# Kernel tuning notes

Measured on AMD Instinct MI355X. Metric: run time of the kernel, lower is better.

Reference implementation:

```python
import jax, jax.numpy as jnp
import numpy as np

CHAN = 24
INNER = 64
GROUPS = 8
M = 5
LAM = 1e-4
MAX_ITER = 25
BETA = 1.0
EPS = 1e-5
B, HH, WW = 128, 32, 32


def conv2d(x, w, b=None):
    # NCHW, OIHW, 3x3 SAME conv (padding = kernel//2)
    y = jax.lax.conv_general_dilated(x, w, (1, 1), 'SAME',
                                     dimension_numbers=('NCHW', 'OIHW', 'NCHW'))
    if b is not None:
        y = y + b[None, :, None, None]
    return y


def group_norm(x, g, b):
    bsz, c, h, w = x.shape
    xg = x.reshape(bsz, GROUPS, c // GROUPS, h, w)
    mu = xg.mean(axis=(2, 3, 4), keepdims=True)
    var = xg.var(axis=(2, 3, 4), keepdims=True)
    xn = ((xg - mu) / jnp.sqrt(var + EPS)).reshape(bsz, c, h, w)
    return xn * g[None, :, None, None] + b[None, :, None, None]


def batch_norm(x, g, b):
    # training-mode batch statistics over (N, H, W)
    mu = x.mean(axis=(0, 2, 3), keepdims=True)
    var = x.var(axis=(0, 2, 3), keepdims=True)
    return (x - mu) / jnp.sqrt(var + EPS) * g[None, :, None, None] + b[None, :, None, None]


def resnet_f(p, z, x):
    c1w, g1g, g1b, c2w, g2g, g2b, g3g, g3b = p
    y = group_norm(jax.nn.relu(conv2d(z, c1w)), g1g, g1b)
    return group_norm(jax.nn.relu(z + group_norm(x + conv2d(y, c2w), g2g, g2b)), g3g, g3b)


def anderson(f, x0):
    # Anderson acceleration, fixed MAX_ITER iterations (no host-sync tol break).
    bsz = x0.shape[0]
    d = x0.size // bsz
    X = jnp.zeros((bsz, M, d), x0.dtype)
    Fm = jnp.zeros((bsz, M, d), x0.dtype)
    f0 = f(x0).reshape(bsz, -1)
    X = X.at[:, 0].set(x0.reshape(bsz, -1))
    Fm = Fm.at[:, 0].set(f0)
    X = X.at[:, 1].set(f0)
    Fm = Fm.at[:, 1].set(f(f0.reshape(x0.shape)).reshape(bsz, -1))
    for k in range(2, MAX_ITER):
        n = min(k, M)
        G = Fm[:, :n] - X[:, :n]                       # [b, n, d]
        Hm = jnp.zeros((bsz, n + 1, n + 1), x0.dtype)
        Hm = Hm.at[:, 0, 1:].set(1.0).at[:, 1:, 0].set(1.0)
        Hm = Hm.at[:, 1:, 1:].set(jnp.einsum('bnd,bmd->bnm', G, G)
                                  + LAM * jnp.eye(n, dtype=x0.dtype)[None])
        yv = jnp.zeros((bsz, n + 1, 1), x0.dtype).at[:, 0, 0].set(1.0)
        alpha = jnp.linalg.solve(Hm, yv)[:, 1:, 0]     # [b, n]
        xnew = (BETA * jnp.einsum('bn,bnd->bd', alpha, Fm[:, :n])
                + (1.0 - BETA) * jnp.einsum('bn,bnd->bd', alpha, X[:, :n]))
        X = X.at[:, k % M].set(xnew)
        Fm = Fm.at[:, k % M].set(f(xnew.reshape(x0.shape)).reshape(bsz, -1))
    return X[:, (MAX_ITER - 1) % M].reshape(x0.shape)


def setup_inputs() -> dict:
    key = jax.random.key(0)
    ks = jax.random.split(key, 8)
    inp = {
        'x': jax.random.normal(ks[0], (B, 3, HH, WW), jnp.float32),
        'pre_conv_w': jax.random.normal(ks[1], (CHAN, 3, 3, 3), jnp.float32) * 0.1,
        'pre_conv_b': jnp.zeros((CHAN,), jnp.float32),
        'pre_bn_g': jnp.ones((CHAN,), jnp.float32),
        'pre_bn_b': jnp.zeros((CHAN,), jnp.float32),
        'f_conv1_w': jax.random.normal(ks[2], (INNER, CHAN, 3, 3), jnp.float32) * 0.01,
        'gn1_g': jnp.ones((INNER,), jnp.float32),
        'gn1_b': jnp.zeros((INNER,), jnp.float32),
        'f_conv2_w': jax.random.normal(ks[3], (CHAN, INNER, 3, 3), jnp.float32) * 0.01,
        'gn2_g': jnp.ones((CHAN,), jnp.float32),
        'gn2_b': jnp.zeros((CHAN,), jnp.float32),
        'gn3_g': jnp.ones((CHAN,), jnp.float32),
        'gn3_b': jnp.zeros((CHAN,), jnp.float32),
        'post_bn_g': jnp.ones((CHAN,), jnp.float32),
        'post_bn_b': jnp.zeros((CHAN,), jnp.float32),
        'fc_w': jax.random.normal(ks[4], (10, CHAN * 4 * 4), jnp.float32) * 0.05,
        'fc_b': jnp.zeros((10,), jnp.float32),
    }
    return inp


def reference(x, pre_conv_w, pre_conv_b, pre_bn_g, pre_bn_b,
              f_conv1_w, gn1_g, gn1_b, f_conv2_w, gn2_g, gn2_b, gn3_g, gn3_b,
              post_bn_g, post_bn_b, fc_w, fc_b):
    # pre: conv + BatchNorm
    xp = batch_norm(conv2d(x, pre_conv_w, pre_conv_b), pre_bn_g, pre_bn_b)
    p = (f_conv1_w, gn1_g, gn1_b, f_conv2_w, gn2_g, gn2_b, gn3_g, gn3_b)
    # DEQ fixed-point solve (eval path: train=False returns the fixed point)
    z_star = anderson(lambda z: resnet_f(p, z, xp), jnp.zeros_like(xp))
    z = resnet_f(p, z_star, xp)
    # post: relu -> BN -> avgpool(8,8) -> flatten -> linear
    h = batch_norm(jax.nn.relu(z), post_bn_g, post_bn_b)
    bsz, c, hh, ww = h.shape
    pooled = h.reshape(bsz, c, hh // 8, 8, ww // 8, 8).mean(axis=(3, 5))  # [B,C,4,4]
    return pooled.reshape(bsz, -1) @ fc_w.T + fc_b
```

## Files before the change

### kernel.cpp

```cpp
#include <hip/hip_runtime.h>
#include <hip/hip_bf16.h>

typedef __hip_bfloat16 bf16;
typedef unsigned short ushortT;
typedef __attribute__((ext_vector_type(8))) short short8;
typedef __attribute__((ext_vector_type(4))) float f32x4;

#define BB 128
#define CHAN 24
#define INNER 64
#define HW 1024
#define DD (CHAN*HW)

constexpr size_t cBD = (size_t)BB*DD;
constexpr size_t cYB = (size_t)BB*INNER*HW;

__device__ __attribute__((aligned(16))) ushortT g_xp[cBD];
__device__ __attribute__((aligned(16))) ushortT g_X[5*cBD];
__device__ __attribute__((aligned(16))) ushortT g_F[5*cBD];
__device__ __attribute__((aligned(16))) ushortT g_G[5*cBD];
__device__ __attribute__((aligned(16))) ushortT g_yb[cYB];
__device__ __attribute__((aligned(16))) ushortT g_tb[cBD];
__device__ __attribute__((aligned(16))) ushortT g_w1m[9*64*32];
__device__ __attribute__((aligned(16))) ushortT g_w2m[9*24*64];
__device__ __attribute__((aligned(16))) float g_stats2a[48];
__device__ __attribute__((aligned(16))) float g_stats2b[48];
__device__ __attribute__((aligned(16))) float g_gn1sum[BB*8*2];
__device__ __attribute__((aligned(16))) float g_gn2sum[BB*24*2];
__device__ __attribute__((aligned(16))) float g_gn3p[BB*4*16];
__device__ __attribute__((aligned(16))) float g_gramp[BB*4*5*5];
__device__ __attribute__((aligned(16))) float g_gram[BB*25];
__device__ __attribute__((aligned(16))) float g_pooled[BB*CHAN*16];
__device__ __attribute__((aligned(16))) float g_params[5120];
__device__ unsigned g_isbf16;

#define P_PCW 0
#define P_PCB 648
#define P_PBG 672
#define P_PBB 696
#define P_G1G 720
#define P_G1B 784
#define P_G2G 848
#define P_G2B 872
#define P_G3G 896
#define P_G3B 920
#define P_POG 944
#define P_POB 968
#define P_FCW 992
#define P_FCB 4832

__device__ __forceinline__ float rdin(const void* p, int i){
  if (g_isbf16) return __bfloat162float(((const bf16*)p)[i]);
  return ((const float*)p)[i];
}
__device__ __forceinline__ float b2f(ushortT u){
  unsigned v = ((unsigned)u) << 16;
  return __builtin_bit_cast(float, v);
}
__device__ __forceinline__ ushortT f2b(float f){
  unsigned u = __builtin_bit_cast(unsigned, f);
  u += 0x7FFFu + ((u >> 16) & 1u);
  return (ushortT)(u >> 16);
}
__device__ __forceinline__ void ld24(const ushortT* p, float* o){
  short8 a = *(const short8*)p, b8 = *(const short8*)(p+8), c8 = *(const short8*)(p+16);
  #pragma unroll
  for (int j=0;j<8;j++){ o[j]=b2f((ushortT)a[j]); o[8+j]=b2f((ushortT)b8[j]); o[16+j]=b2f((ushortT)c8[j]); }
}
__device__ __forceinline__ void st24(ushortT* p, const float* i){
  short8 a,b8,c8;
  #pragma unroll
  for (int j=0;j<8;j++){ a[j]=(short)f2b(i[j]); b8[j]=(short)f2b(i[8+j]); c8[j]=(short)f2b(i[16+j]); }
  *(short8*)p = a; *(short8*)(p+8) = b8; *(short8*)(p+16) = c8;
}

__global__ void detect_k(const void* g1g){
  if (threadIdx.x==0 && blockIdx.x==0){
    unsigned u = *(const unsigned*)g1g;
    g_isbf16 = (u == 0x3F803F80u) ? 1u : 0u;
  }
}

__global__ void cvt_params_k(const void* pcw, const void* pcb, const void* pbg, const void* pbb,
                             const void* g1g, const void* g1b, const void* g2g, const void* g2b,
                             const void* g3g, const void* g3b, const void* pog, const void* pob,
                             const void* fcw, const void* fcb){
  int t = threadIdx.x;
  for (int i=t;i<648;i+=256)  g_params[P_PCW+i]=rdin(pcw,i);
  for (int i=t;i<24;i+=256) { g_params[P_PCB+i]=rdin(pcb,i);
                              g_params[P_PBG+i]=rdin(pbg,i);
                              g_params[P_PBB+i]=rdin(pbb,i);
                              g_params[P_G2G+i]=rdin(g2g,i);
                              g_params[P_G2B+i]=rdin(g2b,i);
                              g_params[P_G3G+i]=rdin(g3g,i);
                              g_params[P_G3B+i]=rdin(g3b,i);
                              g_params[P_POG+i]=rdin(pog,i);
                              g_params[P_POB+i]=rdin(pob,i); }
  for (int i=t;i<64;i+=256) { g_params[P_G1G+i]=rdin(g1g,i);
                              g_params[P_G1B+i]=rdin(g1b,i); }
  for (int i=t;i<3840;i+=256) g_params[P_FCW+i]=rdin(fcw,i);
  for (int i=t;i<10;i+=256)   g_params[P_FCB+i]=rdin(fcb,i);
  for (int i=t;i<48;i+=256) { g_stats2a[i]=0.f; g_stats2b[i]=0.f; }
}

__global__ void wtm_k(const void* w1, const void* w2){
  int t = blockIdx.x*256 + threadIdx.x;
  if (t < 9*64*32){
    int ic = t & 31, oc = (t>>5)&63, s9 = t>>11;
    float v = (ic<24) ? rdin(w1, (oc*24+ic)*9 + s9) : 0.f;
    g_w1m[t] = f2b(v);
  }
  int u = t - 9*64*32;
  if (u >= 0 && u < 9*24*64){
    int ic = u & 63; int rest = u >> 6; int oc = rest % 24; int s9 = rest / 24;
    g_w2m[u] = f2b(rdin(w2, (oc*64+ic)*9 + s9));
  }
}

__global__ void zeroX0_k(){
  size_t i = ((size_t)blockIdx.x*256 + threadIdx.x)*8;
  short8 z = {0,0,0,0,0,0,0,0};
  *(short8*)&g_X[i] = z;
  if (blockIdx.x < 8) g_gn1sum[blockIdx.x*256 + threadIdx.x] = 0.f;
}
__global__ void copyF0toX1_k(){
  size_t i = ((size_t)blockIdx.x*256 + threadIdx.x)*8;
  *(short8*)&g_X[cBD + i] = *(const short8*)&g_F[i];
  if (blockIdx.x < 8) g_gn1sum[blockIdx.x*256 + threadIdx.x] = 0.f;
}

__global__ void preconv_k(const void* __restrict__ x){
  int id = blockIdx.x*256 + threadIdx.x;
  int b = id >> 10, pix = id & 1023;
  int yy = pix >> 5, xx = pix & 31;
  float acc[24];
  #pragma unroll
  for (int oc=0;oc<24;oc++) acc[oc] = g_params[P_PCB+oc];
  for (int ic=0; ic<3; ic++)
    for (int ky=0; ky<3; ky++){
      int gy = yy+ky-1; if (gy<0||gy>=32) continue;
      for (int kx=0;kx<3;kx++){
        int gx = xx+kx-1; if (gx<0||gx>=32) continue;
        float v = rdin(x, ((b*3+ic)*32+gy)*32+gx);
        #pragma unroll
        for (int oc=0;oc<24;oc++)
          acc[oc] += v * g_params[P_PCW+(oc*3+ic)*9+ky*3+kx];
      }
    }
  st24(g_tb + (size_t)id*24, acc);
}

template<bool RELU>
__global__ void bnstat2_k(int which){
  const ushortT* src = (which==0) ? g_tb : (g_F + 4*cBD);
  float* dst = (which==0) ? g_stats2a : g_stats2b;
  __shared__ float sRed[48];
  int b = blockIdx.x >> 2, seg = blockIdx.x & 3;
  int t = threadIdx.x;
  if (t < 48) sRed[t] = 0.f;
  __syncthreads();
  int c8 = t % 3, pl = t / 3;
  float p0[8], p1[8];
  #pragma unroll
  for (int e=0;e<8;e++){ p0[e]=0.f; p1[e]=0.f; }
  for (int it=0; it<4; it++){
    int pix = seg*256 + it*64 + pl;
    short8 v = *(const short8*)&src[((size_t)b*1024 + pix)*24 + c8*8];
    #pragma unroll
    for (int e=0;e<8;e++){
      float f = b2f((ushortT)v[e]); if (RELU) f = fmaxf(f,0.f);
      p0[e]+=f; p1[e]+=f*f;
    }
  }
  #pragma unroll
  for (int e=0;e<8;e++){
    atomicAdd(&sRed[(c8*8+e)*2],   p0[e]);
    atomicAdd(&sRed[(c8*8+e)*2+1], p1[e]);
  }
  __syncthreads();
  if (t < 48) atomicAdd(&dst[t], sRed[t]);
}

__global__ void bn_apply_k(){
  int id = blockIdx.x*256+threadIdx.x;
  const float inv = 1.f/(BB*HW);
  float tv[24], ov[24];
  ld24(g_tb + (size_t)id*24, tv);
  #pragma unroll
  for (int c=0;c<24;c++){
    float mean = g_stats2a[c*2]*inv;
    float var = fmaxf(g_stats2a[c*2+1]*inv - mean*mean, 0.f);
    float rstd = rsqrtf(var + 1e-5f);
    ov[c] = (tv[c]-mean)*rstd*g_params[P_PBG+c] + g_params[P_PBB+c];
  }
  st24(g_xp + (size_t)id*24, ov);
}

__launch_bounds__(256, 2)
__global__ void conv1_k(int s){
  __shared__ ushortT sMem[29312];
  ushortT* sA = sMem;
  ushortT* sW = sMem + 10880;
  const int tid = threadIdx.x;
  const int lane = tid & 63, wv = tid >> 6;
  const int mLane = lane & 15, q = lane >> 4;
  const int b = blockIdx.x >> 2, yt = blockIdx.x & 3;
  const ushortT* __restrict__ Xs = g_X + (size_t)s*cBD;
  if (blockIdx.x < 24) g_gn2sum[blockIdx.x*256 + tid] = 0.f;
  for (int i = tid; i < 1360; i += 256){
    int icv = i & 3, apix = i >> 2;
    int yl = apix / 34, xl = apix - yl*34;
    int gy = yt*8 - 1 + yl, gx = xl - 1;
    short8 v = {0,0,0,0,0,0,0,0};
    if (gy >= 0 && gy < 32 && gx >= 0 && gx < 32 && icv < 3)
      v = *(const short8*)&Xs[((size_t)b*1024 + gy*32 + gx)*24 + icv*8];
    *(short8*)&sA[(size_t)(apix*4 + (icv ^ (apix&3)))*8] = v;
  }
  for (int i = tid; i < 2304; i += 256){
    int icv = i & 3, rest = i >> 2;
    int oc = rest & 63, s9 = rest >> 6;
    short8 v = *(const short8*)&g_w1m[(size_t)((s9*64 + oc)*32) + icv*8];
    *(short8*)&sW[(size_t)((s9*64+oc)*4 + (icv ^ (oc&3)))*8] = v;
  }
  __syncthreads();
  f32x4 acc[4][4];
  #pragma unroll
  for (int mt=0;mt<4;mt++)
    #pragma unroll
    for (int nt=0;nt<4;nt++) acc[mt][nt] = (f32x4){0.f,0.f,0.f,0.f};
  for (int s9=0; s9<9; s9++){
    int ky = s9/3, kx = s9 - ky*3;
    short8 bfr[4];
    #pragma unroll
    for (int nt=0;nt<4;nt++){
      int oc = nt*16 + mLane;
      bfr[nt] = *(const short8*)&sW[(size_t)((s9*64+oc)*4 + (q ^ (oc&3)))*8];
    }
    #pragma unroll
    for (int mt=0;mt<4;mt++){
      int g = wv*4+mt;
      int apix = ((g>>1) + ky)*34 + (g&1)*16 + mLane + kx;
      short8 afr = *(const short8*)&sA[(size_t)(apix*4 + (q ^ (apix&3)))*8];
      #pragma unroll
      for (int nt=0;nt<4;nt++)
        acc[mt][nt] = __builtin_amdgcn_mfma_f32_16x16x32_bf16(afr, bfr[nt], acc[mt][nt], 0,0,0);
    }
  }
  __syncthreads();
  ushortT* sOut = sMem;
  #pragma unroll
  for (int mt=0;mt<4;mt++){
    int g = wv*4+mt;
    #pragma unroll
    for (int nt=0;nt<4;nt++){
      int oc = nt*16 + mLane;
      #pragma unroll
      for (int r=0;r<4;r++){
        int pix = (g>>1)*32 + (g&1)*16 + q*4 + r;
        sOut[pix*64 + oc] = f2b(fmaxf(acc[mt][nt][r], 0.f));
      }
    }
  }
  __syncthreads();
  float s0=0.f, s1=0.f;
  size_t gbase = ((size_t)b*1024 + yt*256)*64;
  for (int c = tid; c < 2048; c += 256){
    short8 v = *(const short8*)&sOut[c*8];
    *(short8*)&g_yb[gbase + (size_t)c*8] = v;
    #pragma unroll
    for (int j=0;j<8;j++){ float f = b2f((ushortT)v[j]); s0 += f; s1 += f*f; }
  }
  s0 += __shfl_down(s0,32); s1 += __shfl_down(s1,32);
  s0 += __shfl_down(s0,16); s1 += __shfl_down(s1,16);
  s0 += __shfl_down(s0, 8); s1 += __shfl_down(s1, 8);
  if (lane < 8){
    atomicAdd(&g_gn1sum[(b*8+lane)*2],   s0);
    atomicAdd(&g_gn1sum[(b*8+lane)*2+1], s1);
  }
}

__launch_bounds__(256, 2)
__global__ void conv2_k(){
  __shared__ ushortT sMem[35584];
  __shared__ float sAff[128];
  ushortT* sA = sMem;
  ushortT* sW = sMem + 21760;
  const int tid = threadIdx.x;
  const int lane = tid & 63, wv = tid >> 6;
  const int mLane = lane & 15, q = lane >> 4;
  const int b = blockIdx.x >> 2, yt = blockIdx.x & 3;
  if (tid < 64){
    int c = tid, gr = c>>3;
    float S = g_gn1sum[(b*8+gr)*2], Q = g_gn1sum[(b*8+gr)*2+1];
    float mean = S*(1.f/8192.f);
    float var = fmaxf(Q*(1.f/8192.f) - mean*mean, 0.f);
    float rstd = rsqrtf(var + 1e-5f);
    float sc = rstd*g_params[P_G1G+c];
    sAff[c] = sc; sAff[64+c] = g_params[P_G1B+c] - mean*sc;
  }
  __syncthreads();
  for (int i = tid; i < 2720; i += 256){
    int icv = i & 7, apix = i >> 3;
    int yl = apix / 34, xl = apix - yl*34;
    int gy = yt*8 - 1 + yl, gx = xl - 1;
    short8 v = {0,0,0,0,0,0,0,0};
    if (gy >= 0 && gy < 32 && gx >= 0 && gx < 32){
      short8 raw = *(const short8*)&g_yb[((size_t)b*1024 + gy*32+gx)*64 + icv*8];
      #pragma unroll
      for (int j=0;j<8;j++){
        int c = icv*8+j;
        v[j] = (short)f2b(b2f((ushortT)raw[j])*sAff[c] + sAff[64+c]);
      }
    }
    *(short8*)&sA[(size_t)(apix*8 + (icv ^ (apix&7)))*8] = v;
  }
  for (int i = tid; i < 1728; i += 256){
    int icv = i & 7, rest = i >> 3;
    int oc = rest % 24, s9 = rest / 24;
    short8 v = *(const short8*)&g_w2m[(size_t)((s9*24+oc)*64) + icv*8];
    *(short8*)&sW[(size_t)((s9*24+oc)*8 + (icv ^ (oc&7)))*8] = v;
  }
  __syncthreads();
  f32x4 acc[4][2];
  #pragma unroll
  for (int mt=0;mt<4;mt++){ acc[mt][0]=(f32x4){0.f,0.f,0.f,0.f}; acc[mt][1]=(f32x4){0.f,0.f,0.f,0.f}; }
  const bool nt1ok = (mLane < 8);
  for (int s9=0; s9<9; s9++){
    int ky = s9/3, kx = s9 - ky*3;
    #pragma unroll
    for (int ks=0; ks<2; ks++){
      int ib = ks*4;
      short8 bfr[2];
      { int oc = mLane;
        bfr[0] = *(const short8*)&sW[(size_t)((s9*24+oc)*8 + ((ib+q) ^ (oc&7)))*8]; }
      if (nt1ok){
        int oc = 16 + mLane;
        bfr[1] = *(const short8*)&sW[(size_t)((s9*24+oc)*8 + ((ib+q) ^ (oc&7)))*8];
      } else bfr[1] = (short8){0,0,0,0,0,0,0,0};
      #pragma unroll
      for (int mt=0;mt<4;mt++){
        int g = wv*4+mt;
        int apix = ((g>>1) + ky)*34 + (g&1)*16 + mLane + kx;
        short8 afr = *(const short8*)&sA[(size_t)(apix*8 + ((ib+q) ^ (apix&7)))*8];
        acc[mt][0] = __builtin_amdgcn_mfma_f32_16x16x32_bf16(afr, bfr[0], acc[mt][0], 0,0,0);
        acc[mt][1] = __builtin_amdgcn_mfma_f32_16x16x32_bf16(afr, bfr[1], acc[mt][1], 0,0,0);
      }
    }
  }
  #pragma unroll
  for (int nt=0;nt<2;nt++){
    int oc = nt*16 + mLane;
    bool ok = (oc < 24);
    float s0=0.f, s1=0.f;
    if (ok){
      #pragma unroll
      for (int mt=0;mt<4;mt++){
        int g = wv*4+mt;
        #pragma unroll
        for (int r=0;r<4;r++){
          int pix = (yt*8 + (g>>1))*32 + (g&1)*16 + q*4 + r;
          size_t o = ((size_t)b*1024 + pix)*24 + oc;
          float v = acc[mt][nt][r] + b2f(g_xp[o]);
          g_tb[o] = f2b(v);
          s0 += v; s1 += v*v;
        }
      }
    }
    s0 += __shfl_down(s0,32); s1 += __shfl_down(s1,32);
    s0 += __shfl_down(s0,16); s1 += __shfl_down(s1,16);
    if (lane < 16 && ok){
      atomicAdd(&g_gn2sum[(b*24+oc)*2],   s0);
      atomicAdd(&g_gn2sum[(b*24+oc)*2+1], s1);
    }
  }
}

__launch_bounds__(256)
__global__ void fuse_a_k(int s){
  __shared__ float sM2[8], sR2[8], sSc2[24], sSb2[24];
  __shared__ float sRed[64];
  const int b = blockIdx.x>>2, seg = blockIdx.x&3;
  const int t = threadIdx.x;
  if (t < 8){
    float S = g_gn2sum[(b*24+t*3)*2]   + g_gn2sum[(b*24+t*3+1)*2]   + g_gn2sum[(b*24+t*3+2)*2];
    float Q = g_gn2sum[(b*24+t*3)*2+1] + g_gn2sum[(b*24+t*3+1)*2+1] + g_gn2sum[(b*24+t*3+2)*2+1];
    float m = S*(1.f/3072.f);
    sM2[t] = m;
    sR2[t] = rsqrtf(fmaxf(Q*(1.f/3072.f) - m*m, 0.f) + 1e-5f);
  }
  __syncthreads();
  if (t < 24){
    int g = t/3;
    float sc = sR2[g]*g_params[P_G2G+t];
    sSc2[t] = sc; sSb2[t] = g_params[P_G2B+t] - sM2[g]*sc;
  }
  __syncthreads();
  size_t pbase = ((size_t)b*1024 + seg*256 + t)*24;
  float tv[24], xv[24];
  ld24(g_tb + pbase, tv);
  ld24(g_X + (size_t)s*cBD + pbase, xv);
  float p0[8], p1[8];
  #pragma unroll
  for (int g=0;g<8;g++){ p0[g]=0.f; p1[g]=0.f; }
  #pragma unroll
  for (int c=0;c<24;c++){
    int g = c/3;
    float v = fmaxf(xv[c] + tv[c]*sSc2[c] + sSb2[c], 0.f);
    p0[g] += v; p1[g] += v*v;
  }
  #pragma unroll
  for (int g=0;g<8;g++){
    for (int off=32;off>0;off>>=1){ p0[g]+=__shfl_down(p0[g],off,64); p1[g]+=__shfl_down(p1[g],off,64); }
  }
  int lane = t&63, wv = t>>6;
  if (lane==0){
    #pragma unroll
    for (int g=0;g<8;g++){ sRed[wv*16+g*2]=p0[g]; sRed[wv*16+g*2+1]=p1[g]; }
  }
  __syncthreads();
  if (t < 16){
    g_gn3p[(b*4+seg)*16 + t] = sRed[t]+sRed[16+t]+sRed[32+t]+sRed[48+t];
  }
}

__launch_bounds__(256)
__global__ void fuse_b_k(int s, int nv){
  __shared__ float sM2[8], sR2[8], sM3[8], sR3[8];
  __shared__ float sSc2[24], sSb2[24], sSc3[24], sSb3[24];
  __shared__ float sRedG[4][5];
  const int b = blockIdx.x>>2, seg = blockIdx.x&3;
  const int t = threadIdx.x;
  if (t < 8){
    float S = g_gn2sum[(b*24+t*3)*2]   + g_gn2sum[(b*24+t*3+1)*2]   + g_gn2sum[(b*24+t*3+2)*2];
    float Q = g_gn2sum[(b*24+t*3)*2+1] + g_gn2sum[(b*24+t*3+1)*2+1] + g_gn2sum[(b*24+t*3+2)*2+1];
    float m = S*(1.f/3072.f);
    sM2[t] = m;
    sR2[t] = rsqrtf(fmaxf(Q*(1.f/3072.f) - m*m, 0.f) + 1e-5f);
    float S3 = g_gn3p[(b*4+0)*16+t*2]   + g_gn3p[(b*4+1)*16+t*2]
             + g_gn3p[(b*4+2)*16+t*2]   + g_gn3p[(b*4+3)*16+t*2];
    float Q3 = g_gn3p[(b*4+0)*16+t*2+1] + g_gn3p[(b*4+1)*16+t*2+1]
             + g_gn3p[(b*4+2)*16+t*2+1] + g_gn3p[(b*4+3)*16+t*2+1];
    float m3 = S3*(1.f/3072.f);
    sM3[t] = m3;
    sR3[t] = rsqrtf(fmaxf(Q3*(1.f/3072.f) - m3*m3, 0.f) + 1e-5f);
  }
  __syncthreads();
  if (t < 24){
    int g = t/3;
    float sc2 = sR2[g]*g_params[P_G2G+t];
    sSc2[t] = sc2; sSb2[t] = g_params[P_G2B+t] - sM2[g]*sc2;
    float sc3 = sR3[g]*g_params[P_G3G+t];
    sSc3[t] = sc3; sSb3[t] = g_params[P_G3B+t] - sM3[g]*sc3;
  }
  __syncthreads();
  size_t pbase = ((size_t)b*1024 + seg*256 + t)*24;
  float tv[24], xv[24], fv[24], gl[24];
  ld24(g_tb + pbase, tv);
  ld24(g_X + (size_t)s*cBD + pbase, xv);
  #pragma unroll
  for (int c=0;c<24;c++){
    float v = fmaxf(xv[c] + tv[c]*sSc2[c] + sSb2[c], 0.f);
    fv[c] = v*sSc3[c] + sSb3[c];
    float g = fv[c] - xv[c];
    gl[c] = b2f(f2b(g));
  }
  st24(g_F + (size_t)s*cBD + pbase, fv);
  st24(g_G + (size_t)s*cBD + pbase, gl);
  if (nv == 0) return;
  float part[5];
  #pragma unroll
  for (int j=0;j<5;j++) part[j]=0.f;
  #pragma unroll
  for (int j=0;j<5;j++){
    if (j>=nv) continue;
    float acc=0.f;
    if (j==s){
      #pragma unroll
      for (int c=0;c<24;c++) acc += gl[c]*gl[c];
    } else {
      float gv[24];
      ld24(g_G + (size_t)j*cBD + pbase, gv);
      #pragma unroll
      for (int c=0;c<24;c++) acc += gl[c]*gv[c];
    }
    part[j]=acc;
  }
  int lane = t&63, wv = t>>6;
  #pragma unroll
  for (int j=0;j<5;j++){
    float v = part[j];
    for (int off=32;off>0;off>>=1) v += __shfl_down(v,off,64);
    if (lane==0 && j<nv) sRedG[wv][j] = v;
  }
  __syncthreads();
  if (t < 5 && t < nv){
    float v = sRedG[0][t]+sRedG[1][t]+sRedG[2][t]+sRedG[3][t];
    g_gramp[((b*4+seg)*5 + s)*5 + t] = v;
  }
}

template<int N>
__device__ __forceinline__ void chol_alpha(const float Kf[5][5], float* alpha){
  double K[N][N];
  #pragma unroll
  for (int i=0;i<N;i++)
    #pragma unroll
    for (int j=0;j<N;j++)
      K[i][j] = (double)Kf[i][j] + (i==j ? 1e-4 : 0.0);
  #pragma unroll
  for (int c=0;c<N;c++){
    double d = K[c][c];
    #pragma unroll
    for (int k2=0;k2<c;k2++) d -= K[c][k2]*K[c][k2];
    d = sqrt(fmax(d, 1e-300));
    K[c][c] = d;
    double inv = 1.0/d;
    #pragma unroll
    for (int r=c+1;r<N;r++){
      double v = K[r][c];
      #pragma unroll
      for (int k2=0;k2<c;k2++) v -= K[r][k2]*K[c][k2];
      K[r][c] = v*inv;
    }
  }
  double y[N];
  #pragma unroll
  for (int i=0;i<N;i++){
    double v = 1.0;
    #pragma unroll
    for (int j=0;j<i;j++) v -= K[i][j]*y[j];
    y[i] = v / K[i][i];
  }
  double w[N];
  #pragma unroll
  for (int i=N-1;i>=0;i--){
    double v = y[i];
    #pragma unroll
    for (int j=i+1;j<N;j++) v -= K[j][i]*w[j];
    w[i] = v / K[i][i];
  }
  double sum = 0.0;
  #pragma unroll
  for (int i=0;i<N;i++) sum += w[i];
  double invs = 1.0/sum;
  #pragma unroll
  for (int i=0;i<N;i++) alpha[i] = (float)(w[i]*invs);
}

__global__ void xns_k(int s, int n, int rA, int nvA, int rB, int nvB){
  __shared__ float sAlpha[5];
  if (blockIdx.x < 8) g_gn1sum[blockIdx.x*256 + threadIdx.x] = 0.f;
  const int b = blockIdx.x >> 2, ch = blockIdx.x & 3;
  const int t = threadIdx.x;
  if (t == 0){
    float Kf[5][5];
    for (int i=0;i<n;i++)
      for (int j=0;j<n;j++) Kf[i][j] = g_gram[b*25 + i*5 + j];
    for (int j=0;j<nvA;j++){
      float v = g_gramp[((b*4+0)*5 + rA)*5 + j] + g_gramp[((b*4+1)*5 + rA)*5 + j]
              + g_gramp[((b*4+2)*5 + rA)*5 + j] + g_gramp[((b*4+3)*5 + rA)*5 + j];
      Kf[rA][j] = v; Kf[j][rA] = v;
    }
    if (rB >= 0){
      for (int j=0;j<nvB;j++){
        float v = g_gramp[((b*4+0)*5 + rB)*5 + j] + g_gramp[((b*4+1)*5 + rB)*5 + j]
                + g_gramp[((b*4+2)*5 + rB)*5 + j] + g_gramp[((b*4+3)*5 + rB)*5 + j];
        Kf[rB][j] = v; Kf[j][rB] = v;
      }
    }
    if (ch == 0){
      for (int j=0;j<nvA;j++){ g_gram[b*25+rA*5+j]=Kf[rA][j]; g_gram[b*25+j*5+rA]=Kf[rA][j]; }
      if (rB >= 0)
        for (int j=0;j<nvB;j++){ g_gram[b*25+rB*5+j]=Kf[rB][j]; g_gram[b*25+j*5+rB]=Kf[rB][j]; }
    }
    float al[5];
    if (n==2) chol_alpha<2>(Kf, al);
    else if (n==3) chol_alpha<3>(Kf, al);
    else if (n==4) chol_alpha<4>(Kf, al);
    else chol_alpha<5>(Kf, al);
    for (int j=0;j<n;j++) sAlpha[j] = al[j];
  }
  __syncthreads();
  float a[5];
  for (int j=0;j<n;j++) a[j] = sAlpha[j];
  const size_t base = (size_t)b*DD + (size_t)ch*6144;
  #pragma unroll
  for (int i=0;i<3;i++){
    size_t off = base + (size_t)i*2048 + (size_t)t*8;
    float acc[8];
    #pragma unroll
    for (int e=0;e<8;e++) acc[e]=0.f;
    for (int j=0;j<n;j++){
      short8 f = *(const short8*)&g_F[(size_t)j*cBD + off];
      float aj = a[j];
      #pragma unroll
      for (int e=0;e<8;e++) acc[e] += aj*b2f((ushortT)f[e]);
    }
    short8 o;
    #pragma unroll
    for (int e=0;e<8;e++) o[e] = (short)f2b(acc[e]);
    *(short8*)&g_X[(size_t)s*cBD + off] = o;
  }
}

__global__ void post_pool_k(){
  int i = blockIdx.x*256+threadIdx.x; if (i >= BB*CHAN*16) return;
  const ushortT* z = g_F + 4*cBD;
  int pw = i&3, ph=(i>>2)&3, c=(i>>4)%CHAN, bi=i/(CHAN*16);
  float inv = 1.f/(BB*HW);
  float mean = g_stats2b[c*2]*inv;
  float var = fmaxf(g_stats2b[c*2+1]*inv - mean*mean, 0.f);
  float rstd = rsqrtf(var + 1e-5f);
  float gg=g_params[P_POG+c], bv=g_params[P_POB+c];
  float s=0.f;
  for (int dy=0;dy<8;dy++)
    for (int dx=0;dx<8;dx++){
      float v = fmaxf(b2f(z[((size_t)bi*1024 + (ph*8+dy)*32 + pw*8+dx)*24 + c]), 0.f);
      s += (v-mean)*rstd*gg + bv;
    }
  g_pooled[i] = s*(1.f/64.f);
}

__global__ void fc_k(void* __restrict__ out){
  int i = blockIdx.x*256+threadIdx.x; if (i>=BB*10) return;
  int j=i%10, bi=i/10;
  float s = g_params[P_FCB+j];
  for (int k=0;k<384;k++) s += g_pooled[bi*384+k]*g_params[P_FCW+j*384+k];
  if (g_isbf16) ((bf16*)out)[i] = __float2bfloat16(s);
  else ((float*)out)[i] = s;
}

extern "C" void kernel_launch(void* const* d_in, const int* in_sizes, int n_in,
                              void* d_out, int out_size, void* d_ws, size_t ws_size,
                              hipStream_t stream){
  const void* x   = d_in[0];
  const void* pcw = d_in[1];
  const void* pcb = d_in[2];
  const void* pbg = d_in[3];
  const void* pbb = d_in[4];
  const void* w1  = d_in[5];
  const void* g1g = d_in[6];
  const void* g1b = d_in[7];
  const void* w2  = d_in[8];
  const void* g2g = d_in[9];
  const void* g2b = d_in[10];
  const void* g3g = d_in[11];
  const void* g3b = d_in[12];
  const void* pog = d_in[13];
  const void* pob = d_in[14];
  const void* fcw = d_in[15];
  const void* fcb = d_in[16];
  (void)d_ws; (void)ws_size;

  const int gPix = (int)(BB*HW/256);

  auto feval = [&](int s, int nv){
    conv1_k<<<512,256,0,stream>>>(s);
    conv2_k<<<512,256,0,stream>>>();
    fuse_a_k<<<512,256,0,stream>>>(s);
    fuse_b_k<<<512,256,0,stream>>>(s, nv);
  };

  detect_k<<<1,64,0,stream>>>(g1g);
  cvt_params_k<<<1,256,0,stream>>>(pcw,pcb,pbg,pbb,g1g,g1b,g2g,g2b,g3g,g3b,pog,pob,fcw,fcb);
  wtm_k<<<126,256,0,stream>>>(w1, w2);

  preconv_k<<<gPix,256,0,stream>>>(x);
  bnstat2_k<false><<<512,192,0,stream>>>(0);
  bn_apply_k<<<gPix,256,0,stream>>>();

  zeroX0_k<<<1536,256,0,stream>>>();
  feval(0, 1);
  copyF0toX1_k<<<1536,256,0,stream>>>();
  feval(1, 2);

  for (int k=2;k<25;k++){
    int n = k<5 ? k : 5;
    int s = k%5;
    int nv = (k+1<5)?(k+1):5;
    if (k==2) xns_k<<<512,256,0,stream>>>(s, 2, 0, 1, 1, 2);
    else      xns_k<<<512,256,0,stream>>>(s, n, (k-1)%5, n, -1, 0);
    feval(s, (k<24) ? nv : 0);
  }

  bnstat2_k<true><<<512,192,0,stream>>>(1);
  post_pool_k<<<(BB*CHAN*16+255)/256,256,0,stream>>>();
  fc_k<<<(BB*10+255)/256,256,0,stream>>>(d_out);
}
```

Measured before the change: 1.650 ms.

## Switch activation layout from NHWC to blocked channel-group-of-8 planes

Activation buffers change from pixel-major with 24 interleaved channels to a [B][3][HW][8] blocked layout, and every kernel's loads and stores are rewritten to match. Each 16-byte short8 access now reads consecutive pixels within one 8-channel group, so neighbouring threads touch contiguous memory instead of 48-byte strides. Some elementwise kernels now issue three separated loads per pixel, and the partially shown code may contain other index paths (such as the Anderson mix kernel) that still assume the old layout.

```diff
diff --git a/kernel.cpp b/kernel.cpp
--- a/kernel.cpp
+++ b/kernel.cpp
@@ -49,6 +49,9 @@
 #define P_FCW 992
 #define P_FCB 4832
 
+__device__ __forceinline__ size_t aidx(int b, int icv, int pix){
+  return (((size_t)b*3 + icv)*1024 + (size_t)pix)*8;
+}
 __device__ __forceinline__ float rdin(const void* p, int i){
   if (g_isbf16) return __bfloat162float(((const bf16*)p)[i]);
   return ((const float*)p)[i];
@@ -62,16 +65,22 @@
   u += 0x7FFFu + ((u >> 16) & 1u);
   return (ushortT)(u >> 16);
 }
-__device__ __forceinline__ void ld24(const ushortT* p, float* o){
-  short8 a = *(const short8*)p, b8 = *(const short8*)(p+8), c8 = *(const short8*)(p+16);
-  #pragma unroll
-  for (int j=0;j<8;j++){ o[j]=b2f((ushortT)a[j]); o[8+j]=b2f((ushortT)b8[j]); o[16+j]=b2f((ushortT)c8[j]); }
-}
-__device__ __forceinline__ void st24(ushortT* p, const float* i){
-  short8 a,b8,c8;
-  #pragma unroll
-  for (int j=0;j<8;j++){ a[j]=(short)f2b(i[j]); b8[j]=(short)f2b(i[8+j]); c8[j]=(short)f2b(i[16+j]); }
-  *(short8*)p = a; *(short8*)(p+8) = b8; *(short8*)(p+16) = c8;
+__device__ __forceinline__ void ld24c(const ushortT* base, int b, int pix, float* o){
+  #pragma unroll
+  for (int icv=0;icv<3;icv++){
+    short8 v = *(const short8*)&base[aidx(b,icv,pix)];
+    #pragma unroll
+    for (int j=0;j<8;j++) o[icv*8+j] = b2f((ushortT)v[j]);
+  }
+}
+__device__ __forceinline__ void st24c(ushortT* base, int b, int pix, const float* i){
+  #pragma unroll
+  for (int icv=0;icv<3;icv++){
+    short8 v;
+    #pragma unroll
+    for (int j=0;j<8;j++) v[j] = (short)f2b(i[icv*8+j]);
+    *(short8*)&base[aidx(b,icv,pix)] = v;
+  }
 }
 
 __global__ void detect_k(const void* g1g){
@@ -147,7 +156,7 @@
           acc[oc] += v * g_params[P_PCW+(oc*3+ic)*9+ky*3+kx];
       }
     }
-  st24(g_tb + (size_t)id*24, acc);
+  st24c(g_tb, b, pix, acc);
 }
 
 template<bool RELU>
@@ -159,13 +168,13 @@
   int t = threadIdx.x;
   if (t < 48) sRed[t] = 0.f;
   __syncthreads();
-  int c8 = t % 3, pl = t / 3;
+  int icv = t >> 6, pl = t & 63;
   float p0[8], p1[8];
   #pragma unroll
   for (int e=0;e<8;e++){ p0[e]=0.f; p1[e]=0.f; }
   for (int it=0; it<4; it++){
     int pix = seg*256 + it*64 + pl;
-    short8 v = *(const short8*)&src[((size_t)b*1024 + pix)*24 + c8*8];
+    short8 v = *(const short8*)&src[aidx(b,icv,pix)];
     #pragma unroll
     for (int e=0;e<8;e++){
       float f = b2f((ushortT)v[e]); if (RELU) f = fmaxf(f,0.f);
@@ -174,8 +183,8 @@
   }
   #pragma unroll
   for (int e=0;e<8;e++){
-    atomicAdd(&sRed[(c8*8+e)*2],   p0[e]);
-    atomicAdd(&sRed[(c8*8+e)*2+1], p1[e]);
+    atomicAdd(&sRed[(icv*8+e)*2],   p0[e]);
+    atomicAdd(&sRed[(icv*8+e)*2+1], p1[e]);
   }
   __syncthreads();
   if (t < 48) atomicAdd(&dst[t], sRed[t]);
@@ -183,9 +192,10 @@
 
 __global__ void bn_apply_k(){
   int id = blockIdx.x*256+threadIdx.x;
+  int b = id >> 10, pix = id & 1023;
   const float inv = 1.f/(BB*HW);
   float tv[24], ov[24];
-  ld24(g_tb + (size_t)id*24, tv);
+  ld24c(g_tb, b, pix, tv);
   #pragma unroll
   for (int c=0;c<24;c++){
     float mean = g_stats2a[c*2]*inv;
@@ -193,7 +203,7 @@
     float rstd = rsqrtf(var + 1e-5f);
     ov[c] = (tv[c]-mean)*rstd*g_params[P_PBG+c] + g_params[P_PBB+c];
   }
-  st24(g_xp + (size_t)id*24, ov);
+  st24c(g_xp, b, pix, ov);
 }
 
 __launch_bounds__(256, 2)
@@ -213,7 +223,7 @@
     int gy = yt*8 - 1 + yl, gx = xl - 1;
     short8 v = {0,0,0,0,0,0,0,0};
     if (gy >= 0 && gy < 32 && gx >= 0 && gx < 32 && icv < 3)
-      v = *(const short8*)&Xs[((size_t)b*1024 + gy*32 + gx)*24 + icv*8];
+      v = *(const short8*)&Xs[aidx(b, icv, gy*32 + gx)];
     *(short8*)&sA[(size_t)(apix*4 + (icv ^ (apix&3)))*8] = v;
   }
   for (int i = tid; i < 2304; i += 256){
@@ -351,6 +361,7 @@
   for (int nt=0;nt<2;nt++){
     int oc = nt*16 + mLane;
     bool ok = (oc < 24);
+    int icv = oc >> 3, e = oc & 7;
     float s0=0.f, s1=0.f;
     if (ok){
       #pragma unroll
@@ -359,7 +370,7 @@
         #pragma unroll
         for (int r=0;r<4;r++){
           int pix = (yt*8 + (g>>1))*32 + (g&1)*16 + q*4 + r;
-          size_t o = ((size_t)b*1024 + pix)*24 + oc;
+          size_t o = aidx(b, icv, pix) + e;
           float v = acc[mt][nt][r] + b2f(g_xp[o]);
           g_tb[o] = f2b(v);
           s0 += v; s1 += v*v;
@@ -395,10 +406,10 @@
     sSc2[t] = sc; sSb2[t] = g_params[P_G2B+t] - sM2[g]*sc;
   }
   __syncthreads();
-  size_t pbase = ((size_t)b*1024 + seg*256 + t)*24;
+  const int pix = seg*256 + t;
   float tv[24], xv[24];
-  ld24(g_tb + pbase, tv);
-  ld24(g_X + (size_t)s*cBD + pbase, xv);
+  ld24c(g_tb, b, pix, tv);
+  ld24c(g_X + (size_t)s*cBD, b, pix, xv);
   float p0[8], p1[8];
   #pragma unroll
   for (int g=0;g<8;g++){ p0[g]=0.f; p1[g]=0.f; }
@@ -453,10 +464,10 @@
     sSc3[t] = sc3; sSb3[t] = g_params[P_G3B+t] - sM3[g]*sc3;
   }
   __syncthreads();
-  size_t pbase = ((size_t)b*1024 + seg*256 + t)*24;
+  const int pix = seg*256 + t;
   float tv[24], xv[24], fv[24], gl[24];
-  ld24(g_tb + pbase, tv);
-  ld24(g_X + (size_t)s*cBD + pbase, xv);
+  ld24c(g_tb, b, pix, tv);
+  ld24c(g_X + (size_t)s*cBD, b, pix, xv);
   #pragma unroll
   for (int c=0;c<24;c++){
     float v = fmaxf(xv[c] + tv[c]*sSc2[c] + sSb2[c], 0.f);
@@ -464,8 +475,8 @@
     float g = fv[c] - xv[c];
     gl[c] = b2f(f2b(g));
   }
-  st24(g_F + (size_t)s*cBD + pbase, fv);
-  st24(g_G + (size_t)s*cBD + pbase, gl);
+  st24c(g_F + (size_t)s*cBD, b, pix, fv);
+  st24c(g_G + (size_t)s*cBD, b, pix, gl);
   if (nv == 0) return;
   float part[5];
   #pragma unroll
@@ -479,7 +490,7 @@
       for (int c=0;c<24;c++) acc += gl[c]*gl[c];
     } else {
       float gv[24];
-      ld24(g_G + (size_t)j*cBD + pbase, gv);
+      ld24c(g_G + (size_t)j*cBD, b, pix, gv);
       #pragma unroll
       for (int c=0;c<24;c++) acc += gl[c]*gv[c];
     }
@@ -607,6 +618,7 @@
   int i = blockIdx.x*256+threadIdx.x; if (i >= BB*CHAN*16) return;
   const ushortT* z = g_F + 4*cBD;
   int pw = i&3, ph=(i>>2)&3, c=(i>>4)%CHAN, bi=i/(CHAN*16);
+  int icv = c>>3, e = c&7;
   float inv = 1.f/(BB*HW);
   float mean = g_stats2b[c*2]*inv;
   float var = fmaxf(g_stats2b[c*2+1]*inv - mean*mean, 0.f);
@@ -615,7 +627,8 @@
   float s=0.f;
   for (int dy=0;dy<8;dy++)
     for (int dx=0;dx<8;dx++){
-      float v = fmaxf(b2f(z[((size_t)bi*1024 + (ph*8+dy)*32 + pw*8+dx)*24 + c]), 0.f);
+      int pix = (ph*8+dy)*32 + pw*8+dx;
+      float v = fmaxf(b2f(z[aidx(bi,icv,pix) + e]), 0.f);
       s += (v-mean)*rstd*gg + bv;
     }
   g_pooled[i] = s*(1.f/64.f);
```

Result: faster. 1.592 ms (-3.5%).
